# Kernel tuning notes

Measured on AMD Instinct MI355X. Metric: run time of the kernel, lower is better.

Reference implementation:

```python
import jax, jax.numpy as jnp
import numpy as np

N, E = 50000, 800000
IN_CH, OUT_CH = 128, 16
H1, D1 = 2, 2 * OUT_CH           # conv1: heads=2, per-head dim 32, concat -> 64
MID = H1 * D1                    # 64
NEG_SLOPE = 0.2

def setup_inputs() -> dict:
    key = jax.random.key(0)
    ks = jax.random.split(key, 16)
    s = lambda k, shape: jax.random.normal(k, shape, dtype=jnp.float32) * 0.1
    return {
        "x": jax.random.normal(ks[0], (N, IN_CH), dtype=jnp.float32),
        "edge_index": jax.random.randint(ks[1], (2, E), 0, N, dtype=jnp.int64),
        "W1": s(ks[2], (IN_CH, H1 * D1)),
        "att_src1": s(ks[3], (H1, D1)),
        "att_dst1": s(ks[4], (H1, D1)),
        "b1": jnp.zeros((MID,), jnp.float32),
        "W_mu": s(ks[5], (MID, OUT_CH)),
        "att_src_mu": s(ks[6], (1, OUT_CH)),
        "att_dst_mu": s(ks[7], (1, OUT_CH)),
        "b_mu": jnp.zeros((OUT_CH,), jnp.float32),
        "W_ls": s(ks[8], (MID, OUT_CH)),
        "att_src_ls": s(ks[9], (1, OUT_CH)),
        "att_dst_ls": s(ks[10], (1, OUT_CH)),
        "b_ls": jnp.zeros((OUT_CH,), jnp.float32),
    }

def gat_conv(x, src, dst, W, att_src, att_dst, bias, heads, d):
    # x: [N, F]; src/dst: [E'] (self loops included); PyG GATConv, eval mode (dropout off)
    n = x.shape[0]
    h = (x @ W).reshape(n, heads, d)                     # [N, H, D]
    a_src = jnp.sum(h * att_src, axis=-1)                # [N, H]
    a_dst = jnp.sum(h * att_dst, axis=-1)                # [N, H]
    e = jax.nn.leaky_relu(a_src[src] + a_dst[dst], NEG_SLOPE)   # [E', H]
    # segment softmax over incoming edges of each destination node
    m = jax.ops.segment_max(e, dst, num_segments=n)
    ex = jnp.exp(e - m[dst])
    denom = jax.ops.segment_sum(ex, dst, num_segments=n)
    alpha = ex / (denom[dst] + 1e-16)                    # [E', H]
    msg = h[src] * alpha[:, :, None]                     # [E', H, D]
    out = jax.ops.segment_sum(msg, dst, num_segments=n)  # [N, H, D]
    return out, bias

def reference(x, edge_index, W1, att_src1, att_dst1, b1,
              W_mu, att_src_mu, att_dst_mu, b_mu,
              W_ls, att_src_ls, att_dst_ls, b_ls):
    n = x.shape[0]
    loops = jnp.arange(n, dtype=edge_index.dtype)
    src = jnp.concatenate([edge_index[0], loops])        # add_self_loops=True (inputs have none)
    dst = jnp.concatenate([edge_index[1], loops])
    h, b = gat_conv(x, src, dst, W1, att_src1, att_dst1, b1, H1, D1)
    h = jax.nn.relu(h.reshape(n, H1 * D1) + b)           # concat=True -> [N, 64]
    mu, bm = gat_conv(h, src, dst, W_mu, att_src_mu, att_dst_mu, b_mu, 1, OUT_CH)
    ls, bl = gat_conv(h, src, dst, W_ls, att_src_ls, att_dst_ls, b_ls, 1, OUT_CH)
    mu = mu.mean(axis=1) + bm                            # concat=False, heads=1 -> mean == squeeze
    ls = ls.mean(axis=1) + bl
    return (mu, ls)
```

## Files before the change

### kernel.cpp

```cpp
#include <hip/hip_runtime.h>

#define NEG 0.2f

typedef __attribute__((ext_vector_type(8))) short short8;
typedef __attribute__((ext_vector_type(4))) float f32x4;

__device__ __forceinline__ float lrelu(float v) { return v > 0.f ? v : NEG * v; }

__device__ __forceinline__ unsigned short f2bf(float f) {
    unsigned u = __float_as_uint(f);
    unsigned r = (u + 0x7FFF + ((u >> 16) & 1)) >> 16;
    return (unsigned short)r;
}
__device__ __forceinline__ float bf2f(unsigned short h) { return __uint_as_float((unsigned)h << 16); }
__device__ __forceinline__ float bf_lo(unsigned v) { return __uint_as_float(v << 16); }
__device__ __forceinline__ float bf_hi(unsigned v) { return __uint_as_float(v & 0xffff0000u); }

__global__ void build_w1ext(const float* __restrict__ W1, const float* __restrict__ asrc,
                            const float* __restrict__ adst,
                            unsigned short* __restrict__ Wt_hi, unsigned short* __restrict__ Wt_lo) {
    int i = blockIdx.x * blockDim.x + threadIdx.x;
    if (i >= 128 * 80) return;
    int k = i / 80, c = i % 80;
    float val;
    if (c < 64) val = W1[k * 64 + c];
    else if (c < 68) {
        int j = c - 64;
        int hh = j & 1;
        const float* att = (j >= 2) ? adst : asrc;
        float s = 0.f;
        for (int d = 0; d < 32; ++d) s += W1[k * 64 + hh * 32 + d] * att[hh * 32 + d];
        val = s;
    } else val = 0.f;
    unsigned short h = f2bf(val);
    Wt_hi[c * 128 + k] = h;
    Wt_lo[c * 128 + k] = f2bf(val - bf2f(h));
}

__global__ void build_w2ext(const float* __restrict__ Wmu, const float* __restrict__ Wls,
                            const float* __restrict__ asmu, const float* __restrict__ admu,
                            const float* __restrict__ asls, const float* __restrict__ adls,
                            unsigned short* __restrict__ Wt_hi, unsigned short* __restrict__ Wt_lo) {
    int i = blockIdx.x * blockDim.x + threadIdx.x;
    if (i >= 64 * 48) return;
    int k = i / 48, c = i % 48;
    float val;
    if (c < 16) val = Wmu[k * 16 + c];
    else if (c < 32) val = Wls[k * 16 + (c - 16)];
    else if (c < 36) {
        int j = c - 32;
        const float* W = (j < 2) ? Wmu : Wls;
        const float* att = (j == 0) ? asmu : (j == 1) ? admu : (j == 2) ? asls : adls;
        float s = 0.f;
        for (int c2 = 0; c2 < 16; ++c2) s += W[k * 16 + c2] * att[c2];
        val = s;
    } else val = 0.f;
    unsigned short h = f2bf(val);
    Wt_hi[c * 64 + k] = h;
    Wt_lo[c * 64 + k] = f2bf(val - bf2f(h));
}

__global__ __launch_bounds__(256) void gemm1(const float* __restrict__ x,
                                             const unsigned short* __restrict__ Wt_hi,
                                             const unsigned short* __restrict__ Wt_lo,
                                             unsigned short* __restrict__ hbf,
                                             float* __restrict__ a1, int n) {
    int wid = threadIdx.x >> 6, lane = threadIdx.x & 63;
    int m = lane & 15, b = lane >> 4;
    int row = blockIdx.x * 64 + wid * 16 + m;
    int rowc = min(row, n - 1);
    short8 ah[4], al[4];
    const float* xp = x + (size_t)rowc * 128 + b * 8;
#pragma unroll
    for (int kc = 0; kc < 4; ++kc) {
        float4 v0 = *(const float4*)(xp + kc * 32);
        float4 v1 = *(const float4*)(xp + kc * 32 + 4);
        float vv[8] = {v0.x, v0.y, v0.z, v0.w, v1.x, v1.y, v1.z, v1.w};
#pragma unroll
        for (int j = 0; j < 8; ++j) {
            unsigned short h = f2bf(vv[j]);
            ah[kc][j] = (short)h;
            al[kc][j] = (short)f2bf(vv[j] - bf2f(h));
        }
    }
    int orow0 = blockIdx.x * 64 + wid * 16 + b * 4;
#pragma unroll
    for (int ct = 0; ct < 5; ++ct) {
        f32x4 acc = {0.f, 0.f, 0.f, 0.f};
        int col = ct * 16 + m;
        const unsigned short* wh = Wt_hi + col * 128 + b * 8;
        const unsigned short* wl = Wt_lo + col * 128 + b * 8;
#pragma unroll
        for (int kc = 0; kc < 4; ++kc) {
            short8 bh = *(const short8*)(wh + kc * 32);
            short8 bl = *(const short8*)(wl + kc * 32);
            acc = __builtin_amdgcn_mfma_f32_16x16x32_bf16(ah[kc], bh, acc, 0, 0, 0);
            acc = __builtin_amdgcn_mfma_f32_16x16x32_bf16(al[kc], bh, acc, 0, 0, 0);
            acc = __builtin_amdgcn_mfma_f32_16x16x32_bf16(ah[kc], bl, acc, 0, 0, 0);
        }
        if (ct < 4) {
#pragma unroll
            for (int j = 0; j < 4; ++j) {
                int orow = orow0 + j;
                if (orow < n) hbf[(size_t)orow * 64 + ct * 16 + m] = f2bf(acc[j]);
            }
        } else if (m < 4) {
#pragma unroll
            for (int j = 0; j < 4; ++j) {
                int orow = orow0 + j;
                if (orow < n) a1[(size_t)orow * 4 + m] = acc[j];
            }
        }
    }
}

__global__ __launch_bounds__(256) void gemm2(const unsigned short* __restrict__ h1bf,
                                             const unsigned short* __restrict__ Wt_hi,
                                             const unsigned short* __restrict__ Wt_lo,
                                             unsigned* __restrict__ hml, float* __restrict__ a2, int n) {
    int wid = threadIdx.x >> 6, lane = threadIdx.x & 63;
    int m = lane & 15, b = lane >> 4;
    int row = blockIdx.x * 64 + wid * 16 + m;
    int rowc = min(row, n - 1);
    short8 a0 = *(const short8*)(h1bf + (size_t)rowc * 64 + b * 8);
    short8 a1f = *(const short8*)(h1bf + (size_t)rowc * 64 + 32 + b * 8);
    int orow0 = blockIdx.x * 64 + wid * 16 + b * 4;
    f32x4 accs[3];
#pragma unroll
    for (int ct = 0; ct < 3; ++ct) {
        f32x4 acc = {0.f, 0.f, 0.f, 0.f};
        int col = ct * 16 + m;
        const unsigned short* wh = Wt_hi + col * 64 + b * 8;
        const unsigned short* wl = Wt_lo + col * 64 + b * 8;
        short8 bh0 = *(const short8*)(wh);
        short8 bl0 = *(const short8*)(wl);
        short8 bh1 = *(const short8*)(wh + 32);
        short8 bl1 = *(const short8*)(wl + 32);
        acc = __builtin_amdgcn_mfma_f32_16x16x32_bf16(a0, bh0, acc, 0, 0, 0);
        acc = __builtin_amdgcn_mfma_f32_16x16x32_bf16(a0, bl0, acc, 0, 0, 0);
        acc = __builtin_amdgcn_mfma_f32_16x16x32_bf16(a1f, bh1, acc, 0, 0, 0);
        acc = __builtin_amdgcn_mfma_f32_16x16x32_bf16(a1f, bl1, acc, 0, 0, 0);
        accs[ct] = acc;
    }
#pragma unroll
    for (int j = 0; j < 4; ++j) {
        int orow = orow0 + j;
        if (orow >= n) break;
        hml[(size_t)orow * 16 + m] = ((unsigned)f2bf(accs[1][j]) << 16) | f2bf(accs[0][j]);
        if (m < 4) a2[(size_t)orow * 4 + m] = accs[2][j];
    }
}

__global__ __launch_bounds__(256) void count_deg_part(const int* __restrict__ dstv, int E, int np,
                                                      int* __restrict__ deg) {
    int p = blockIdx.x & 7;
    int bslot = blockIdx.x >> 3;
    int nblk = gridDim.x >> 3;
    int lo = p * np, hi = lo + np;
    for (int i = bslot * 256 + threadIdx.x; i < E; i += nblk * 256) {
        int d = dstv[i];
        if (d >= lo && d < hi) atomicAdd(&deg[d], 1);
    }
}

__global__ __launch_bounds__(256) void scatter_part(const int* __restrict__ srcv,
                                                    const int* __restrict__ dstv, int E, int np,
                                                    int* __restrict__ cursor, int* __restrict__ srcs) {
    int p = blockIdx.x & 7;
    int bslot = blockIdx.x >> 3;
    int nblk = gridDim.x >> 3;
    int lo = p * np, hi = lo + np;
    for (int i = bslot * 256 + threadIdx.x; i < E; i += nblk * 256) {
        int d = dstv[i];
        if (d >= lo && d < hi) {
            int slot = atomicAdd(&cursor[d], 1);
            srcs[slot] = srcv[i];
        }
    }
}

__global__ __launch_bounds__(256) void block_sums(const int* __restrict__ deg, int n,
                                                  int* __restrict__ bsums) {
    int i = blockIdx.x * 256 + threadIdx.x;
    int v = (i < n) ? deg[i] : 0;
    for (int o = 32; o > 0; o >>= 1) v += __shfl_down(v, o, 64);
    __shared__ int ws[4];
    if ((threadIdx.x & 63) == 0) ws[threadIdx.x >> 6] = v;
    __syncthreads();
    if (threadIdx.x == 0) bsums[blockIdx.x] = ws[0] + ws[1] + ws[2] + ws[3];
}

__global__ __launch_bounds__(256) void scan_bsums(int* __restrict__ bsums, int nb) {
    __shared__ int s[256];
    int t = threadIdx.x;
    int v = (t < nb) ? bsums[t] : 0;
    s[t] = v;
    __syncthreads();
    for (int o = 1; o < 256; o <<= 1) {
        int u = (t >= o) ? s[t - o] : 0;
        __syncthreads();
        s[t] += u;
        __syncthreads();
    }
    if (t < nb) bsums[t] = s[t] - v;
}

__global__ __launch_bounds__(256) void write_offs(const int* __restrict__ deg,
                                                  const int* __restrict__ bsums, int n,
                                                  int* __restrict__ offs, int* __restrict__ cursor) {
    int t = threadIdx.x;
    int i = blockIdx.x * 256 + t;
    int v = (i < n) ? deg[i] : 0;
    __shared__ int s[256];
    s[t] = v;
    __syncthreads();
    for (int o = 1; o < 256; o <<= 1) {
        int u = (t >= o) ? s[t - o] : 0;
        __syncthreads();
        s[t] += u;
        __syncthreads();
    }
    int excl = s[t] - v + bsums[blockIdx.x];
    if (i < n) { offs[i] = excl; cursor[i] = excl; }
    if (i == n - 1) offs[n] = excl + v;
}

__global__ __launch_bounds__(256) void agg1(const unsigned* __restrict__ h32, const float* __restrict__ a1,
                                            const int* __restrict__ offs, const int* __restrict__ srcs,
                                            const float* __restrict__ b1, unsigned* __restrict__ h1u, int n) {
    int wid = threadIdx.x >> 6, lane = threadIdx.x & 63;
    int node = blockIdx.x * 4 + wid;
    if (node >= n) return;
    int q = lane >> 4;
    int l = lane & 15;
    int head = l >> 3;
    float adst = a1[node * 4 + 2 + head];
    float ax = 0.f, ay = 0.f, az = 0.f, aw = 0.f, denom = 0.f;
    if (q == 0) {
        float w = __expf(lrelu(a1[node * 4 + head] + adst));
        uint2 hv = *(const uint2*)&h32[node * 32 + 2 * l];
        ax = w * bf_lo(hv.x); ay = w * bf_hi(hv.x);
        az = w * bf_lo(hv.y); aw = w * bf_hi(hv.y);
        denom = w;
    }
    int kb = offs[node], ke = offs[node + 1];
    for (int k = kb + q; k < ke; k += 4) {
        int s = srcs[k];
        float wv = __expf(lrelu(a1[s * 4 + head] + adst));
        uint2 hv = *(const uint2*)&h32[s * 32 + 2 * l];
        denom += wv;
        ax += wv * bf_lo(hv.x); ay += wv * bf_hi(hv.x);
        az += wv * bf_lo(hv.y); aw += wv * bf_hi(hv.y);
    }
    ax += __shfl_xor(ax, 16, 64); ax += __shfl_xor(ax, 32, 64);
    ay += __shfl_xor(ay, 16, 64); ay += __shfl_xor(ay, 32, 64);
    az += __shfl_xor(az, 16, 64); az += __shfl_xor(az, 32, 64);
    aw += __shfl_xor(aw, 16, 64); aw += __shfl_xor(aw, 32, 64);
    denom += __shfl_xor(denom, 16, 64); denom += __shfl_xor(denom, 32, 64);
    if (q == 0) {
        float4 bv = *(const float4*)&b1[4 * l];
        float o0 = fmaxf(ax / denom + bv.x, 0.f);
        float o1 = fmaxf(ay / denom + bv.y, 0.f);
        float o2 = fmaxf(az / denom + bv.z, 0.f);
        float o3 = fmaxf(aw / denom + bv.w, 0.f);
        uint2 o;
        o.x = ((unsigned)f2bf(o1) << 16) | f2bf(o0);
        o.y = ((unsigned)f2bf(o3) << 16) | f2bf(o2);
        *(uint2*)&h1u[node * 32 + 2 * l] = o;
    }
}

__global__ __launch_bounds__(256) void agg2(const unsigned* __restrict__ hml,
                                            const float* __restrict__ a2, const int* __restrict__ offs,
                                            const int* __restrict__ srcs,
                                            const float* __restrict__ bmu, const float* __restrict__ bls,
                                            float* __restrict__ out, int n) {
    int wid = threadIdx.x >> 6, lane = threadIdx.x & 63;
    int node = blockIdx.x * 4 + wid;
    if (node >= n) return;
    int q = lane >> 4, c = lane & 15;
    float admu = a2[node * 4 + 1], adls = a2[node * 4 + 3];
    float amu = 0.f, als = 0.f, dmu = 0.f, dls = 0.f;
    if (q == 0) {
        float wmu = __expf(lrelu(a2[node * 4 + 0] + admu));
        float wls = __expf(lrelu(a2[node * 4 + 2] + adls));
        unsigned hv = hml[node * 16 + c];
        amu = wmu * bf_lo(hv); als = wls * bf_hi(hv);
        dmu = wmu; dls = wls;
    }
    int kb = offs[node], ke = offs[node + 1];
    for (int k = kb + q; k < ke; k += 4) {
        int s = srcs[k];
        float4 av = *(const float4*)&a2[s * 4];
        float w1v = __expf(lrelu(av.x + admu));
        float w2v = __expf(lrelu(av.z + adls));
        unsigned hv = hml[s * 16 + c];
        dmu += w1v; dls += w2v;
        amu += w1v * bf_lo(hv);
        als += w2v * bf_hi(hv);
    }
    amu += __shfl_xor(amu, 16, 64); amu += __shfl_xor(amu, 32, 64);
    als += __shfl_xor(als, 16, 64); als += __shfl_xor(als, 32, 64);
    dmu += __shfl_xor(dmu, 16, 64); dmu += __shfl_xor(dmu, 32, 64);
    dls += __shfl_xor(dls, 16, 64); dls += __shfl_xor(dls, 32, 64);
    if (q == 0) {
        out[node * 16 + c] = amu / dmu + bmu[c];
        out[(size_t)n * 16 + node * 16 + c] = als / dls + bls[c];
    }
}

extern "C" void kernel_launch(void* const* d_in, const int* in_sizes, int n_in,
                              void* d_out, int out_size, void* d_ws, size_t ws_size,
                              hipStream_t stream) {
    const float* x    = (const float*)d_in[0];
    const int*   ei   = (const int*)d_in[1];
    const float* W1   = (const float*)d_in[2];
    const float* as1  = (const float*)d_in[3];
    const float* ad1  = (const float*)d_in[4];
    const float* b1   = (const float*)d_in[5];
    const float* Wmu  = (const float*)d_in[6];
    const float* asmu = (const float*)d_in[7];
    const float* admu = (const float*)d_in[8];
    const float* bmu  = (const float*)d_in[9];
    const float* Wls  = (const float*)d_in[10];
    const float* asls = (const float*)d_in[11];
    const float* adls = (const float*)d_in[12];
    const float* bls  = (const float*)d_in[13];
    float* out = (float*)d_out;

    int n = in_sizes[0] / 128;
    int E = in_sizes[1] / 2;
    int np = (n + 7) / 8;

    char* ws = (char*)d_ws;
    size_t off = 0;
    auto alloc = [&](size_t b) { size_t p = off; off = (off + b + 255) & ~(size_t)255; return p; };

    unsigned short* hbf  = (unsigned short*)(ws + alloc((size_t)n * 64 * 2));
    unsigned*       h1u  = (unsigned*)(ws + alloc((size_t)n * 32 * 4));
    float*          a1   = (float*)(ws + alloc((size_t)n * 4 * 4));
    unsigned*       hml  = (unsigned*)(ws + alloc((size_t)n * 16 * 4));
    float*          a2   = (float*)(ws + alloc((size_t)n * 4 * 4));
    unsigned short* w1h  = (unsigned short*)(ws + alloc(80 * 128 * 2));
    unsigned short* w1l  = (unsigned short*)(ws + alloc(80 * 128 * 2));
    unsigned short* w2h  = (unsigned short*)(ws + alloc(48 * 64 * 2));
    unsigned short* w2l  = (unsigned short*)(ws + alloc(48 * 64 * 2));
    int*   deg    = (int*)(ws + alloc((size_t)n * 4));
    int*   offs   = (int*)(ws + alloc((size_t)(n + 1) * 4));
    int*   cursor = (int*)(ws + alloc((size_t)n * 4));
    int*   srcs   = (int*)(ws + alloc((size_t)E * 4));
    int*   bsums  = (int*)(ws + alloc(1024 * 4));

    int nb = (n + 255) / 256;

    hipMemsetAsync(deg, 0, (size_t)n * 4, stream);
    build_w1ext<<<(128 * 80 + 255) / 256, 256, 0, stream>>>(W1, as1, ad1, w1h, w1l);
    build_w2ext<<<(64 * 48 + 255) / 256, 256, 0, stream>>>(Wmu, Wls, asmu, admu, asls, adls, w2h, w2l);
    gemm1<<<(n + 63) / 64, 256, 0, stream>>>(x, w1h, w1l, hbf, a1, n);
    count_deg_part<<<2048, 256, 0, stream>>>(ei + E, E, np, deg);
    block_sums<<<nb, 256, 0, stream>>>(deg, n, bsums);
    scan_bsums<<<1, 256, 0, stream>>>(bsums, nb);
    write_offs<<<nb, 256, 0, stream>>>(deg, bsums, n, offs, cursor);
    scatter_part<<<2048, 256, 0, stream>>>(ei, ei + E, E, np, cursor, srcs);
    agg1<<<(n + 3) / 4, 256, 0, stream>>>((const unsigned*)hbf, a1, offs, srcs, b1, h1u, n);
    gemm2<<<(n + 63) / 64, 256, 0, stream>>>((const unsigned short*)h1u, w2h, w2l, hml, a2, n);
    agg2<<<(n + 3) / 4, 256, 0, stream>>>(hml, a2, offs, srcs, bmu, bls, out, n);
}
```

Before: 277.1 us.

## Merge weight-prep and scan kernels, compact source scores, prefetch neighbor indices

Merges the two weight-preparation kernels into one launch and folds the block-sum scan into write_offs, which removes two kernel launches. The GEMMs also write a compact float2 array holding only the source attention scores, so the aggregation gathers 8 bytes per neighbor instead of 16. Both aggregation loops load up to 64 neighbor indices per wave in one coalesced read and hand them out by shuffle instead of reading srcs each iteration. The cost is an extra small array write per node, a redundant 256-element scan repeated in every write_offs block, and masked tail iterations in the edge loop.

Result: slower. 284.2 us (+2.6%).

```diff
diff --git a/kernel.cpp b/kernel.cpp
--- a/kernel.cpp
+++ b/kernel.cpp
@@ -16,55 +16,55 @@
 __device__ __forceinline__ float bf_lo(unsigned v) { return __uint_as_float(v << 16); }
 __device__ __forceinline__ float bf_hi(unsigned v) { return __uint_as_float(v & 0xffff0000u); }
 
-__global__ void build_w1ext(const float* __restrict__ W1, const float* __restrict__ asrc,
-                            const float* __restrict__ adst,
-                            unsigned short* __restrict__ Wt_hi, unsigned short* __restrict__ Wt_lo) {
+__global__ void build_w(const float* __restrict__ W1, const float* __restrict__ as1,
+                        const float* __restrict__ ad1,
+                        const float* __restrict__ Wmu, const float* __restrict__ Wls,
+                        const float* __restrict__ asmu, const float* __restrict__ admu,
+                        const float* __restrict__ asls, const float* __restrict__ adls,
+                        unsigned short* __restrict__ w1h, unsigned short* __restrict__ w1l,
+                        unsigned short* __restrict__ w2h, unsigned short* __restrict__ w2l) {
     int i = blockIdx.x * blockDim.x + threadIdx.x;
-    if (i >= 128 * 80) return;
-    int k = i / 80, c = i % 80;
-    float val;
-    if (c < 64) val = W1[k * 64 + c];
-    else if (c < 68) {
-        int j = c - 64;
-        int hh = j & 1;
-        const float* att = (j >= 2) ? adst : asrc;
-        float s = 0.f;
-        for (int d = 0; d < 32; ++d) s += W1[k * 64 + hh * 32 + d] * att[hh * 32 + d];
-        val = s;
-    } else val = 0.f;
-    unsigned short h = f2bf(val);
-    Wt_hi[c * 128 + k] = h;
-    Wt_lo[c * 128 + k] = f2bf(val - bf2f(h));
-}
-
-__global__ void build_w2ext(const float* __restrict__ Wmu, const float* __restrict__ Wls,
-                            const float* __restrict__ asmu, const float* __restrict__ admu,
-                            const float* __restrict__ asls, const float* __restrict__ adls,
-                            unsigned short* __restrict__ Wt_hi, unsigned short* __restrict__ Wt_lo) {
-    int i = blockIdx.x * blockDim.x + threadIdx.x;
-    if (i >= 64 * 48) return;
-    int k = i / 48, c = i % 48;
-    float val;
-    if (c < 16) val = Wmu[k * 16 + c];
-    else if (c < 32) val = Wls[k * 16 + (c - 16)];
-    else if (c < 36) {
-        int j = c - 32;
-        const float* W = (j < 2) ? Wmu : Wls;
-        const float* att = (j == 0) ? asmu : (j == 1) ? admu : (j == 2) ? asls : adls;
-        float s = 0.f;
-        for (int c2 = 0; c2 < 16; ++c2) s += W[k * 16 + c2] * att[c2];
-        val = s;
-    } else val = 0.f;
-    unsigned short h = f2bf(val);
-    Wt_hi[c * 64 + k] = h;
-    Wt_lo[c * 64 + k] = f2bf(val - bf2f(h));
+    if (i < 128 * 80) {
+        int k = i / 80, c = i % 80;
+        float val;
+        if (c < 64) val = W1[k * 64 + c];
+        else if (c < 68) {
+            int j = c - 64;
+            int hh = j & 1;
+            const float* att = (j >= 2) ? ad1 : as1;
+            float s = 0.f;
+            for (int d = 0; d < 32; ++d) s += W1[k * 64 + hh * 32 + d] * att[hh * 32 + d];
+            val = s;
+        } else val = 0.f;
+        unsigned short h = f2bf(val);
+        w1h[c * 128 + k] = h;
+        w1l[c * 128 + k] = f2bf(val - bf2f(h));
+    } else {
+        int i2 = i - 128 * 80;
+        if (i2 >= 64 * 48) return;
+        int k = i2 / 48, c = i2 % 48;
+        float val;
+        if (c < 16) val = Wmu[k * 16 + c];
+        else if (c < 32) val = Wls[k * 16 + (c - 16)];
+        else if (c < 36) {
+            int j = c - 32;
+            const float* W = (j < 2) ? Wmu : Wls;
+            const float* att = (j == 0) ? asmu : (j == 1) ? admu : (j == 2) ? asls : adls;
+            float s = 0.f;
+            for (int c2 = 0; c2 < 16; ++c2) s += W[k * 16 + c2] * att[c2];
+            val = s;
+        } else val = 0.f;
+        unsigned short h = f2bf(val);
+        w2h[c * 64 + k] = h;
+        w2l[c * 64 + k] = f2bf(val - bf2f(h));
+    }
 }
 
 __global__ __launch_bounds__(256) void gemm1(const float* __restrict__ x,
                                              const unsigned short* __restrict__ Wt_hi,
                                              const unsigned short* __restrict__ Wt_lo,
                                              unsigned short* __restrict__ hbf,
-                                             float* __restrict__ a1, int n) {
+                                             float* __restrict__ a1, float2* __restrict__ a1s, int n) {
     int wid = threadIdx.x >> 6, lane = threadIdx.x & 63;
     int m = lane & 15, b = lane >> 4;
     int row = blockIdx.x * 64 + wid * 16 + m;
@@ -104,11 +104,17 @@
                 int orow = orow0 + j;
                 if (orow < n) hbf[(size_t)orow * 64 + ct * 16 + m] = f2bf(acc[j]);
             }
-        } else if (m < 4) {
+        } else {
+            int base = lane & 48;
 #pragma unroll
             for (int j = 0; j < 4; ++j) {
+                float c0 = __shfl(acc[j], base + 0, 64);
+                float c1 = __shfl(acc[j], base + 1, 64);
                 int orow = orow0 + j;
-                if (orow < n) a1[(size_t)orow * 4 + m] = acc[j];
+                if (orow < n) {
+                    if (m < 4) a1[(size_t)orow * 4 + m] = acc[j];
+                    if (m == 0) a1s[orow] = make_float2(c0, c1);
+                }
             }
         }
     }
@@ -117,7 +123,8 @@
 __global__ __launch_bounds__(256) void gemm2(const unsigned short* __restrict__ h1bf,
                                              const unsigned short* __restrict__ Wt_hi,
                                              const unsigned short* __restrict__ Wt_lo,
-                                             unsigned* __restrict__ hml, float* __restrict__ a2, int n) {
+                                             unsigned* __restrict__ hml, float* __restrict__ a2,
+                                             float2* __restrict__ a2s, int n) {
     int wid = threadIdx.x >> 6, lane = threadIdx.x & 63;
     int m = lane & 15, b = lane >> 4;
     int row = blockIdx.x * 64 + wid * 16 + m;
@@ -142,12 +149,16 @@
         acc = __builtin_amdgcn_mfma_f32_16x16x32_bf16(a1f, bl1, acc, 0, 0, 0);
         accs[ct] = acc;
     }
+    int base = lane & 48;
 #pragma unroll
     for (int j = 0; j < 4; ++j) {
         int orow = orow0 + j;
-        if (orow >= n) break;
+        float c0 = __shfl(accs[2][j], base + 0, 64);
+        float c2 = __shfl(accs[2][j], base + 2, 64);
+        if (orow >= n) continue;
         hml[(size_t)orow * 16 + m] = ((unsigned)f2bf(accs[1][j]) << 16) | f2bf(accs[0][j]);
         if (m < 4) a2[(size_t)orow * 4 + m] = accs[2][j];
+        if (m == 0) a2s[orow] = make_float2(c0, c2);
     }
 }
 
@@ -190,10 +201,24 @@
     if (threadIdx.x == 0) bsums[blockIdx.x] = ws[0] + ws[1] + ws[2] + ws[3];
 }
 
-__global__ __launch_bounds__(256) void scan_bsums(int* __restrict__ bsums, int nb) {
+__global__ __launch_bounds__(256) void write_offs(const int* __restrict__ deg,
+                                                  const int* __restrict__ bsums, int nb, int n,
+                                                  int* __restrict__ offs, int* __restrict__ cursor) {
+    __shared__ int sb[256];
     __shared__ int s[256];
     int t = threadIdx.x;
-    int v = (t < nb) ? bsums[t] : 0;
+    int bv = (t < nb) ? bsums[t] : 0;
+    sb[t] = bv;
+    __syncthreads();
+    for (int o = 1; o < 256; o <<= 1) {
+        int u = (t >= o) ? sb[t - o] : 0;
+        __syncthreads();
+        sb[t] += u;
+        __syncthreads();
+    }
+    int base0 = (blockIdx.x == 0) ? 0 : sb[blockIdx.x - 1];
+    int i = blockIdx.x * 256 + t;
+    int v = (i < n) ? deg[i] : 0;
     s[t] = v;
     __syncthreads();
     for (int o = 1; o < 256; o <<= 1) {
@@ -202,30 +227,13 @@
         s[t] += u;
         __syncthreads();
     }
-    if (t < nb) bsums[t] = s[t] - v;
-}
-
-__global__ __launch_bounds__(256) void write_offs(const int* __restrict__ deg,
-                                                  const int* __restrict__ bsums, int n,
-                                                  int* __restrict__ offs, int* __restrict__ cursor) {
-    int t = threadIdx.x;
-    int i = blockIdx.x * 256 + t;
-    int v = (i < n) ? deg[i] : 0;
-    __shared__ int s[256];
-    s[t] = v;
-    __syncthreads();
-    for (int o = 1; o < 256; o <<= 1) {
-        int u = (t >= o) ? s[t - o] : 0;
-        __syncthreads();
-        s[t] += u;
-        __syncthreads();
-    }
-    int excl = s[t] - v + bsums[blockIdx.x];
+    int excl = s[t] - v + base0;
     if (i < n) { offs[i] = excl; cursor[i] = excl; }
     if (i == n - 1) offs[n] = excl + v;
 }
 
 __global__ __launch_bounds__(256) void agg1(const unsigned* __restrict__ h32, const float* __restrict__ a1,
+                                            const float2* __restrict__ a1s,
                                             const int* __restrict__ offs, const int* __restrict__ srcs,
                                             const float* __restrict__ b1, unsigned* __restrict__ h1u, int n) {
     int wid = threadIdx.x >> 6, lane = threadIdx.x & 63;
@@ -243,10 +251,16 @@
         az = w * bf_lo(hv.y); aw = w * bf_hi(hv.y);
         denom = w;
     }
-    int kb = offs[node], ke = offs[node + 1];
-    for (int k = kb + q; k < ke; k += 4) {
-        int s = srcs[k];
-        float wv = __expf(lrelu(a1[s * 4 + head] + adst));
+    int kb = offs[node];
+    int deg = offs[node + 1] - kb;
+    int pre = (lane < deg) ? srcs[kb + lane] : 0;
+    for (int idx0 = 0; idx0 < deg; idx0 += 4) {
+        int idx = idx0 + q;
+        int idc = min(idx, deg - 1);
+        int s = (idc < 64) ? __shfl(pre, idc, 64) : srcs[kb + idc];
+        float2 ap = a1s[s];
+        float asrc = head ? ap.y : ap.x;
+        float wv = (idx < deg) ? __expf(lrelu(asrc + adst)) : 0.f;
         uint2 hv = *(const uint2*)&h32[s * 32 + 2 * l];
         denom += wv;
         ax += wv * bf_lo(hv.x); ay += wv * bf_hi(hv.x);
@@ -271,8 +285,8 @@
 }
 
 __global__ __launch_bounds__(256) void agg2(const unsigned* __restrict__ hml,
-                                            const float* __restrict__ a2, const int* __restrict__ offs,
-                                            const int* __restrict__ srcs,
+                                            const float* __restrict__ a2, const float2* __restrict__ a2s,
+                                            const int* __restrict__ offs, const int* __restrict__ srcs,
                                             const float* __restrict__ bmu, const float* __restrict__ bls,
                                             float* __restrict__ out, int n) {
     int wid = threadIdx.x >> 6, lane = threadIdx.x & 63;
@@ -288,12 +302,17 @@
         amu = wmu * bf_lo(hv); als = wls * bf_hi(hv);
         dmu = wmu; dls = wls;
     }
-    int kb = offs[node], ke = offs[node + 1];
-    for (int k = kb + q; k < ke; k += 4) {
-        int s = srcs[k];
-        float4 av = *(const float4*)&a2[s * 4];
-        float w1v = __expf(lrelu(av.x + admu));
-        float w2v = __expf(lrelu(av.z + adls));
+    int kb = offs[node];
+    int deg = offs[node + 1] - kb;
+    int pre = (lane < deg) ? srcs[kb + lane] : 0;
+    for (int idx0 = 0; idx0 < deg; idx0 += 4) {
+        int idx = idx0 + q;
+        int idc = min(idx, deg - 1);
+        int s = (idc < 64) ? __shfl(pre, idc, 64) : srcs[kb + idc];
+        float2 ap = a2s[s];
+        bool ok = idx < deg;
+        float w1v = ok ? __expf(lrelu(ap.x + admu)) : 0.f;
+        float w2v = ok ? __expf(lrelu(ap.y + adls)) : 0.f;
         unsigned hv = hml[s * 16 + c];
         dmu += w1v; dls += w2v;
         amu += w1v * bf_lo(hv);
@@ -339,8 +358,10 @@
     unsigned short* hbf  = (unsigned short*)(ws + alloc((size_t)n * 64 * 2));
     unsigned*       h1u  = (unsigned*)(ws + alloc((size_t)n * 32 * 4));
     float*          a1   = (float*)(ws + alloc((size_t)n * 4 * 4));
+    float2*         a1s  = (float2*)(ws + alloc((size_t)n * 8));
     unsigned*       hml  = (unsigned*)(ws + alloc((size_t)n * 16 * 4));
     float*          a2   = (float*)(ws + alloc((size_t)n * 4 * 4));
+    float2*         a2s  = (float2*)(ws + alloc((size_t)n * 8));
     unsigned short* w1h  = (unsigned short*)(ws + alloc(80 * 128 * 2));
     unsigned short* w1l  = (unsigned short*)(ws + alloc(80 * 128 * 2));
     unsigned short* w2h  = (unsigned short*)(ws + alloc(48 * 64 * 2));
@@ -354,15 +375,14 @@
     int nb = (n + 255) / 256;
 
     hipMemsetAsync(deg, 0, (size_t)n * 4, stream);
-    build_w1ext<<<(128 * 80 + 255) / 256, 256, 0, stream>>>(W1, as1, ad1, w1h, w1l);
-    build_w2ext<<<(64 * 48 + 255) / 256, 256, 0, stream>>>(Wmu, Wls, asmu, admu, asls, adls, w2h, w2l);
-    gemm1<<<(n + 63) / 64, 256, 0, stream>>>(x, w1h, w1l, hbf, a1, n);
+    build_w<<<(128 * 80 + 64 * 48 + 255) / 256, 256, 0, stream>>>(W1, as1, ad1, Wmu, Wls, asmu, admu,
+                                                                  asls, adls, w1h, w1l, w2h, w2l);
+    gemm1<<<(n + 63) / 64, 256, 0, stream>>>(x, w1h, w1l, hbf, a1, a1s, n);
     count_deg_part<<<2048, 256, 0, stream>>>(ei + E, E, np, deg);
     block_sums<<<nb, 256, 0, stream>>>(deg, n, bsums);
-    scan_bsums<<<1, 256, 0, stream>>>(bsums, nb);
-    write_offs<<<nb, 256, 0, stream>>>(deg, bsums, n, offs, cursor);
+    write_offs<<<nb, 256, 0, stream>>>(deg, bsums, nb, n, offs, cursor);
     scatter_part<<<2048, 256, 0, stream>>>(ei, ei + E, E, np, cursor, srcs);
-    agg1<<<(n + 3) / 4, 256, 0, stream>>>((const unsigned*)hbf, a1, offs, srcs, b1, h1u, n);
-    gemm2<<<(n + 63) / 64, 256, 0, stream>>>((const unsigned short*)h1u, w2h, w2l, hml, a2, n);
-    agg2<<<(n + 3) / 4, 256, 0, stream>>>(hml, a2, offs, srcs, bmu, bls, out, n);
-}
+    agg1<<<(n + 3) / 4, 256, 0, stream>>>((const unsigned*)hbf, a1, a1s, offs, srcs, b1, h1u, n);
+    gemm2<<<(n + 63) / 64, 256, 0, stream>>>((const unsigned short*)h1u, w2h, w2l, hml, a2, a2s, n);
+    agg2<<<(n + 3) / 4, 256, 0, stream>>>(hml, a2, a2s, offs, srcs, bmu, bls, out, n);
+}
```
